# Performance work log

Hardware: AMD Instinct MI355X
Metric: run time of the kernel (lower is better)

The kernel has to match this reference:

```python
import jax, jax.numpy as jnp
import numpy as np

N, M, K, C, FF, H, OUT = 20000, 80000, 48, 64, 256, 4, 64


def _lin(x, w, b):
    return x @ w.T + b


def _bn(x, g, b, eps=1e-5):
    mu = x.mean(0)
    var = x.var(0)
    return (x - mu) * jax.lax.rsqrt(var + eps) * g + b


def setup_inputs() -> dict:
    key = jax.random.key(0)
    ks = jax.random.split(key, 24)
    voxel_features = jax.random.normal(ks[0], (M, C), jnp.float32)
    voxel_coords = jax.random.normal(ks[1], (M, 3), jnp.float32)
    query_coords = jax.random.normal(ks[2], (N, 3), jnp.float32)
    idx = jax.random.randint(ks[3], (N, K), 0, M)
    drop = jax.random.uniform(ks[4], (N, K)) < 0.1
    drop = drop.at[:, 0].set(False)  # keep >=1 valid key per query
    key_indices = jnp.where(drop, -1, idx)
    s = 0.05
    p = lambda i, shp: jax.random.normal(ks[i], shp, jnp.float32) * s
    return {
        "voxel_features": voxel_features,
        "voxel_coords": voxel_coords,
        "query_coords": query_coords,
        "key_indices": key_indices,
        "q_w": p(5, (C, 3)), "q_b": p(6, (C,)),
        "kpos_w": p(7, (C, 3)), "kpos_b": p(8, (C,)),
        "in_w": p(9, (3 * C, C)), "in_b": p(10, (3 * C,)),
        "out_w": p(11, (C, C)), "out_b": p(12, (C,)),
        "lin1_w": p(13, (FF, C)), "lin1_b": p(14, (FF,)),
        "lin2_w": p(15, (C, FF)), "lin2_b": p(16, (C,)),
        "norm_g": jnp.ones((C,), jnp.float32), "norm_b": jnp.zeros((C,), jnp.float32),
        "outl_w": p(17, (OUT, C)), "outl_b": p(18, (OUT,)),
        "obn_g": jnp.ones((OUT,), jnp.float32), "obn_b": jnp.zeros((OUT,), jnp.float32),
    }


def reference(voxel_features, voxel_coords, query_coords, key_indices,
              q_w, q_b, kpos_w, kpos_b, in_w, in_b, out_w, out_b,
              lin1_w, lin1_b, lin2_w, lin2_b, norm_g, norm_b,
              outl_w, outl_b, obn_g, obn_b):
    hd = C // H
    mask = key_indices < 0                      # (N,K) padded keys
    safe = jnp.where(mask, 0, key_indices)
    key_feats = voxel_features[safe]            # (N,K,C) hash-gather
    key_coords = voxel_coords[safe]             # (N,K,3)
    # query positional projection
    q_feat = jax.nn.relu(_lin(query_coords, q_w, q_b))          # (N,C)
    # relative coords + key positional conv1d(kernel=1) == linear on coord dim
    rel = key_coords - query_coords[:, None, :]                  # (N,K,3)
    key_feats = key_feats + jax.nn.relu(_lin(rel, kpos_w, kpos_b))
    # multihead attention, query length 1 per voxel
    Wq, Wk, Wv = jnp.split(in_w, 3, axis=0)
    bq, bk, bv = jnp.split(in_b, 3)
    q = (_lin(q_feat, Wq, bq) / jnp.sqrt(jnp.float32(hd))).reshape(N, H, hd)
    k = _lin(key_feats, Wk, bk).reshape(N, K, H, hd)
    v = _lin(key_feats, Wv, bv).reshape(N, K, H, hd)
    scores = jnp.einsum('nhd,nkhd->nhk', q, k)
    scores = jnp.where(mask[:, None, :], -jnp.inf, scores)
    attn = jax.nn.softmax(scores, axis=-1)
    ctx = jnp.einsum('nhk,nkhd->nhd', attn, v).reshape(N, C)
    att = _lin(ctx, out_w, out_b)                                # (N,C)
    # FFN + residual
    x = att + _lin(jax.nn.relu(_lin(att, lin1_w, lin1_b)), lin2_w, lin2_b)
    x = _bn(x, norm_g, norm_b)
    # output layer: Linear -> BN -> ReLU
    x = jax.nn.relu(_bn(_lin(x, outl_w, outl_b), obn_g, obn_b))
    return x
```

## Files before the change

### kernel.cpp

```cpp
#include <hip/hip_runtime.h>
#include <math.h>

#define N_Q 20000
#define KK 48
#define CC 64
#define FFD 256

#define TW_WOT   0
#define TW_WVT   4096
#define TW_L1B   8192
#define TW_L2B   16384
#define TW_OLB   24576
#define TW_QB    26624
#define TW_KB    28672
#define ST_OFF   32768
#define M_OFF    33024
#define VF_OFF   2593024

typedef short bf16x8 __attribute__((ext_vector_type(8)));
typedef float f32x4  __attribute__((ext_vector_type(4)));

__device__ __forceinline__ unsigned f2bf(float f) {
    unsigned u = __float_as_uint(f);
    return (u + 0x7fffu + ((u >> 16) & 1u)) >> 16;
}
__device__ __forceinline__ unsigned pk2(float a, float b) {
    return f2bf(a) | (f2bf(b) << 16);
}
__device__ __forceinline__ float bflo(unsigned u) { return __uint_as_float(u << 16); }
__device__ __forceinline__ float bfhi(unsigned u) { return __uint_as_float(u & 0xffff0000u); }
__device__ __forceinline__ bf16x8 ldfrag(const unsigned short* p) {
    return *(const bf16x8*)p;
}

__global__ void prep_all(const float* __restrict__ in_w,
                         const float* __restrict__ out_w,
                         const float* __restrict__ lin1_w,
                         const float* __restrict__ lin2_w,
                         const float* __restrict__ outl_w,
                         const float* __restrict__ vfeat,
                         float* __restrict__ tw,
                         unsigned short* __restrict__ vfeat_bf,
                         float* __restrict__ stats)
{
    int t = blockIdx.x * 256 + threadIdx.x;
    unsigned* twu = (unsigned*)tw;
    if (t < 1280000) {
        float4 v = ((const float4*)vfeat)[t];
        uint2 p; p.x = pk2(v.x, v.y); p.y = pk2(v.z, v.w);
        ((uint2*)vfeat_bf)[t] = p;
    }
    if (t < 256) stats[t] = 0.0f;
    if (t < 4096) {
        int c = t >> 6, j = t & 63;
        tw[TW_WOT + j*64 + c] = out_w[c*64 + j];
    } else if (t < 8192) {
        int i = t - 4096, cp = i >> 6, c = i & 63;
        tw[TW_WVT + cp*64 + c] = in_w[(128 + c)*64 + cp];
    } else if (t < 16384) {
        int p = t - 8192;
        int j2 = p & 3, lane = (p >> 2) & 63, nb = (p >> 8) & 15, ks = p >> 12;
        int n = nb*16 + (lane & 15), k = ks*32 + (lane >> 4)*8 + 2*j2;
        twu[TW_L1B + p] = pk2(lin1_w[n*64 + k], lin1_w[n*64 + k + 1]);
    } else if (t < 24576) {
        int p = t - 16384;
        int j2 = p & 3, lane = (p >> 2) & 63, nb = (p >> 8) & 3, ks = p >> 10;
        int n = nb*16 + (lane & 15), k = ks*32 + (lane >> 4)*8 + 2*j2;
        twu[TW_L2B + p] = pk2(lin2_w[n*256 + k], lin2_w[n*256 + k + 1]);
    } else if (t < 26624) {
        int p = t - 24576;
        int j2 = p & 3, lane = (p >> 2) & 63, nb = (p >> 8) & 3, ks = p >> 10;
        int n = nb*16 + (lane & 15), k = ks*32 + (lane >> 4)*8 + 2*j2;
        twu[TW_OLB + p] = pk2(outl_w[n*64 + k], outl_w[n*64 + k + 1]);
    } else if (t < 28672) {
        int p = t - 26624;
        int j2 = p & 3, lane = (p >> 2) & 63, nb = (p >> 8) & 3, ks = p >> 10;
        int n = nb*16 + (lane & 15), k = ks*32 + (lane >> 4)*8 + 2*j2;
        twu[TW_QB + p] = pk2(in_w[n*64 + k], in_w[n*64 + k + 1]);
    } else if (t < 32768) {
        int p = t - 28672;
        int j2 = p & 3, lane = (p >> 2) & 63, nb = (p >> 8) & 3, h = p >> 10;
        int j = nb*16 + (lane & 15), k = (lane >> 4)*8 + 2*j2;
        unsigned u = 0;
        if (k < 16)
            u = pk2(in_w[(64 + h*16 + k)*64 + j], in_w[(64 + h*16 + k + 1)*64 + j]);
        twu[TW_KB + p] = u;
    }
}

__global__ __launch_bounds__(256) void m_kernel(
    const float* __restrict__ qcoord, const float* __restrict__ q_w,
    const float* __restrict__ q_b, const float* __restrict__ in_b,
    const float* __restrict__ tw, unsigned short* __restrict__ M_all)
{
    __shared__ __align__(16) unsigned short sQF[80*72];
    __shared__ __align__(16) unsigned short sQ[80*72];
    int t = threadIdx.x, base = blockIdx.x * 80;
    int colq = (t*4) & 63;
    float qwv[12];
    #pragma unroll
    for (int j = 0; j < 12; ++j) qwv[j] = q_w[colq*3 + j];
    float4 qb4 = *(const float4*)&q_b[colq];
    #pragma unroll
    for (int i = 0; i < 5; ++i) {
        int e = i*1024 + t*4, r = e >> 6, n = base + r;
        float c0 = qcoord[n*3], c1 = qcoord[n*3+1], c2 = qcoord[n*3+2];
        float f0 = fmaxf(fmaf(qwv[2],  c2, fmaf(qwv[1],  c1, fmaf(qwv[0], c0, qb4.x))), 0.f);
        float f1 = fmaxf(fmaf(qwv[5],  c2, fmaf(qwv[4],  c1, fmaf(qwv[3], c0, qb4.y))), 0.f);
        float f2 = fmaxf(fmaf(qwv[8],  c2, fmaf(qwv[7],  c1, fmaf(qwv[6], c0, qb4.z))), 0.f);
        float f3 = fmaxf(fmaf(qwv[11], c2, fmaf(qwv[10], c1, fmaf(qwv[9], c0, qb4.w))), 0.f);
        uint2 p; p.x = pk2(f0, f1); p.y = pk2(f2, f3);
        *(uint2*)&sQF[r*72 + colq] = p;
    }
    int w = t >> 6, lane = t & 63, l16 = lane & 15, quad = lane >> 4;
    const unsigned* QB = (const unsigned*)(tw + TW_QB);
    const unsigned* KB = (const unsigned*)(tw + TW_KB);
    bf16x8 qbf[2], kbf[4];
    #pragma unroll
    for (int ks = 0; ks < 2; ++ks)
        qbf[ks] = ldfrag((const unsigned short*)&QB[((ks*4 + w)*64 + lane)*4]);
    #pragma unroll
    for (int nb = 0; nb < 4; ++nb)
        kbf[nb] = ldfrag((const unsigned short*)&KB[((w*4 + nb)*64 + lane)*4]);
    __syncthreads();

    int cq = w*16 + l16;
    float bq = in_b[cq];
    #pragma unroll
    for (int mb = 0; mb < 5; ++mb) {
        bf16x8 a0 = ldfrag(&sQF[(mb*16 + l16)*72 + quad*8]);
        bf16x8 a1 = ldfrag(&sQF[(mb*16 + l16)*72 + 32 + quad*8]);
        f32x4 acc = {0.f, 0.f, 0.f, 0.f};
        acc = __builtin_amdgcn_mfma_f32_16x16x32_bf16(a0, qbf[0], acc, 0, 0, 0);
        acc = __builtin_amdgcn_mfma_f32_16x16x32_bf16(a1, qbf[1], acc, 0, 0, 0);
        #pragma unroll
        for (int reg = 0; reg < 4; ++reg) {
            int row = mb*16 + quad*4 + reg;
            sQ[row*72 + cq] = (unsigned short)f2bf((acc[reg] + bq) * 0.25f);
        }
    }
    #pragma unroll
    for (int mb = 0; mb < 5; ++mb) {
        bf16x8 a = {0,0,0,0,0,0,0,0};
        if (quad < 2) a = ldfrag(&sQ[(mb*16 + l16)*72 + w*16 + quad*8]);
        f32x4 acc[4];
        #pragma unroll
        for (int nb = 0; nb < 4; ++nb) {
            f32x4 z = {0.f, 0.f, 0.f, 0.f};
            acc[nb] = __builtin_amdgcn_mfma_f32_16x16x32_bf16(a, kbf[nb], z, 0, 0, 0);
        }
        #pragma unroll
        for (int nb = 0; nb < 4; ++nb)
            #pragma unroll
            for (int reg = 0; reg < 4; ++reg) {
                int r = base + mb*16 + quad*4 + reg, j = nb*16 + l16;
                M_all[(size_t)r*256 + j*4 + w] = (unsigned short)f2bf(acc[nb][reg]);
            }
    }
}

__global__ __launch_bounds__(64, 4) void attn_kernel(
    const unsigned short* __restrict__ vfeat_bf, const float* __restrict__ vcoord,
    const float* __restrict__ qcoord, const int* __restrict__ kidx,
    const float* __restrict__ kpos_w, const float* __restrict__ kpos_b,
    const float* __restrict__ in_b, const float* __restrict__ out_b,
    const float* __restrict__ tw, const unsigned short* __restrict__ M_all,
    float* __restrict__ att_out)
{
    __shared__ __align__(16) unsigned short skf[KK*72];
    __shared__ __align__(16) float reg1[256];
    int n = blockIdx.x, c = threadIdx.x;
    int l16 = c & 15, h = c >> 4;
    float* sM   = reg1;
    float* sP   = reg1;
    float* sctx = reg1 + 192;
    float* sT   = (float*)skf;

    {
        uint2 mu = ((const uint2*)(M_all + (size_t)n*256))[c];
        float4 mf;
        mf.x = bflo(mu.x); mf.y = bfhi(mu.x);
        mf.z = bflo(mu.y); mf.w = bfhi(mu.y);
        *(float4*)&sM[4*c] = mf;
    }

    float qc0 = qcoord[n*3+0], qc1 = qcoord[n*3+1], qc2 = qcoord[n*3+2];

    int kread = c < 48 ? c : 47;
    int idxv = kidx[(size_t)n*KK + kread];
    int sfe = idxv < 0 ? 0 : idxv;
    float rl0 = vcoord[sfe*3+0] - qc0;
    float rl1 = vcoord[sfe*3+1] - qc1;
    float rl2 = vcoord[sfe*3+2] - qc2;

    float4 wA  = *(const float4*)(kpos_w + 12*l16 + 0);
    float4 wB  = *(const float4*)(kpos_w + 12*l16 + 4);
    float4 wC  = *(const float4*)(kpos_w + 12*l16 + 8);
    float4 kb4 = *(const float4*)(kpos_b + 4*l16);

    uint2 fv[12];
    #pragma unroll
    for (int i = 0; i < 12; ++i) {
        int row = 4*i + h;
        int si = __shfl(idxv, row);
        si = si < 0 ? 0 : si;
        fv[i] = *(const uint2*)(vfeat_bf + (size_t)si*64 + 4*l16);
    }
    #pragma unroll
    for (int i = 0; i < 12; ++i) {
        int row = 4*i + h;
        float rr0 = __shfl(rl0, row), rr1 = __shfl(rl1, row), rr2 = __shfl(rl2, row);
        float g0 = bflo(fv[i].x), g1 = bfhi(fv[i].x);
        float g2 = bflo(fv[i].y), g3 = bfhi(fv[i].y);
        g0 += fmaxf(fmaf(wA.x, rr0, fmaf(wA.y, rr1, fmaf(wA.z, rr2, kb4.x))), 0.0f);
        g1 += fmaxf(fmaf(wA.w, rr0, fmaf(wB.x, rr1, fmaf(wB.y, rr2, kb4.y))), 0.0f);
        g2 += fmaxf(fmaf(wB.z, rr0, fmaf(wB.w, rr1, fmaf(wC.x, rr2, kb4.z))), 0.0f);
        g3 += fmaxf(fmaf(wC.y, rr0, fmaf(wC.z, rr1, fmaf(wC.w, rr2, kb4.w))), 0.0f);
        uint2 p; p.x = pk2(g0, g1); p.y = pk2(g2, g3);
        *(uint2*)&skf[row*72 + 4*l16] = p;
    }

    int i0 = __shfl(idxv, l16), i1 = __shfl(idxv, l16 + 16), i2 = __shfl(idxv, l16 + 32);
    float S0 = 0, S1 = 0, S2 = 0;
    #pragma unroll
    for (int j8 = 0; j8 < 8; ++j8) {
        uint2 A = *(const uint2*)&skf[ l16       *72 + 8*j8];
        uint2 A2= *(const uint2*)&skf[ l16       *72 + 8*j8 + 4];
        uint2 B = *(const uint2*)&skf[(l16 + 16) *72 + 8*j8];
        uint2 B2= *(const uint2*)&skf[(l16 + 16) *72 + 8*j8 + 4];
        uint2 D = *(const uint2*)&skf[(l16 + 32) *72 + 8*j8];
        uint2 D2= *(const uint2*)&skf[(l16 + 32) *72 + 8*j8 + 4];
        #pragma unroll
        for (int jj = 0; jj < 8; ++jj) {
            unsigned ua = (jj < 4) ? ((jj < 2) ? A.x : A.y) : ((jj < 6) ? A2.x : A2.y);
            unsigned ub = (jj < 4) ? ((jj < 2) ? B.x : B.y) : ((jj < 6) ? B2.x : B2.y);
            unsigned ud = (jj < 4) ? ((jj < 2) ? D.x : D.y) : ((jj < 6) ? D2.x : D2.y);
            float av = (jj & 1) ? bfhi(ua) : bflo(ua);
            float bv = (jj & 1) ? bfhi(ub) : bflo(ub);
            float dv = (jj & 1) ? bfhi(ud) : bflo(ud);
            float m  = sM[(8*j8 + jj)*4 + h];
            S0 = fmaf(av, m, S0);
            S1 = fmaf(bv, m, S1);
            S2 = fmaf(dv, m, S2);
        }
    }
    if (i0 < 0) S0 = -INFINITY;
    if (i1 < 0) S1 = -INFINITY;
    if (i2 < 0) S2 = -INFINITY;

    float mx = fmaxf(S0, fmaxf(S1, S2));
    #pragma unroll
    for (int off = 8; off >= 1; off >>= 1) mx = fmaxf(mx, __shfl_xor(mx, off, 16));
    float e0 = __expf(S0 - mx), e1 = __expf(S1 - mx), e2 = __expf(S2 - mx);
    float es = e0 + e1 + e2;
    #pragma unroll
    for (int off = 8; off >= 1; off >>= 1) es += __shfl_xor(es, off, 16);
    float rinv = 1.0f / es;
    sP[ l16       *4 + h] = e0 * rinv;
    sP[(l16 + 16) *4 + h] = e1 * rinv;
    sP[(l16 + 32) *4 + h] = e2 * rinv;

    float T0 = 0, T1 = 0, T2 = 0, T3 = 0;
    #pragma unroll 8
    for (int k = 0; k < KK; ++k) {
        float kf = __uint_as_float(((unsigned)skf[k*72 + c]) << 16);
        float4 p = *(const float4*)&sP[k*4];
        T0 = fmaf(p.x, kf, T0); T1 = fmaf(p.y, kf, T1);
        T2 = fmaf(p.z, kf, T2); T3 = fmaf(p.w, kf, T3);
    }
    sT[0*65 + c] = T0; sT[1*65 + c] = T1; sT[2*65 + c] = T2; sT[3*65 + c] = T3;

    const float* WvT = tw + TW_WVT;
    float ctx = in_b[128 + c];
    #pragma unroll 8
    for (int cp = 0; cp < 64; ++cp)
        ctx = fmaf(sT[h*65 + cp], WvT[cp*64 + c], ctx);
    sctx[c] = ctx;

    const float* WoT = tw + TW_WOT;
    float att = out_b[c];
    #pragma unroll 8
    for (int j = 0; j < 64; ++j)
        att = fmaf(sctx[j], WoT[j*64 + c], att);
    att_out[(size_t)n*64 + c] = att;
}

__global__ __launch_bounds__(256) void ffn_kernel(
    const float* __restrict__ tw, const float* __restrict__ lin1_b,
    const float* __restrict__ lin2_b, float* __restrict__ att_y,
    float* __restrict__ sum1, float* __restrict__ sumsq1)
{
    __shared__ __align__(16) unsigned short sA[80*72];
    __shared__ __align__(16) unsigned short sH[80*264];
    int t = threadIdx.x, base = blockIdx.x * 80;
    #pragma unroll
    for (int i = 0; i < 5; ++i) {
        int e = i*1024 + t*4, r = e >> 6, col = e & 63;
        float4 v = *(const float4*)&att_y[(size_t)(base + r)*64 + col];
        uint2 p; p.x = pk2(v.x, v.y); p.y = pk2(v.z, v.w);
        *(uint2*)&sA[r*72 + col] = p;
    }
    int w = t >> 6, lane = t & 63, l16 = lane & 15, quad = lane >> 4;
    const unsigned* L1B = (const unsigned*)(tw + TW_L1B);
    const unsigned* L2B = (const unsigned*)(tw + TW_L2B);
    bf16x8 b1f[2][4], b2f[8];
    #pragma unroll
    for (int ks = 0; ks < 2; ++ks)
        #pragma unroll
        for (int nb = 0; nb < 4; ++nb)
            b1f[ks][nb] = ldfrag((const unsigned short*)&L1B[((ks*16 + w*4 + nb)*64 + lane)*4]);
    #pragma unroll
    for (int ks = 0; ks < 8; ++ks)
        b2f[ks] = ldfrag((const unsigned short*)&L2B[((ks*4 + w)*64 + lane)*4]);
    __syncthreads();

    #pragma unroll
    for (int mb = 0; mb < 5; ++mb) {
        bf16x8 a0 = ldfrag(&sA[(mb*16 + l16)*72 + quad*8]);
        bf16x8 a1 = ldfrag(&sA[(mb*16 + l16)*72 + 32 + quad*8]);
        #pragma unroll
        for (int nb = 0; nb < 4; ++nb) {
            f32x4 acc = {0.f, 0.f, 0.f, 0.f};
            acc = __builtin_amdgcn_mfma_f32_16x16x32_bf16(a0, b1f[0][nb], acc, 0, 0, 0);
            acc = __builtin_amdgcn_mfma_f32_16x16x32_bf16(a1, b1f[1][nb], acc, 0, 0, 0);
            int f = w*64 + nb*16 + l16;
            float bias = lin1_b[f];
            #pragma unroll
            for (int reg = 0; reg < 4; ++reg) {
                int row = mb*16 + quad*4 + reg;
                sH[row*264 + f] = (unsigned short)f2bf(fmaxf(acc[reg] + bias, 0.0f));
            }
        }
    }
    __syncthreads();

    int c = w*16 + l16;
    float lb2 = lin2_b[c];
    float s = 0.f, ss = 0.f;
    #pragma unroll
    for (int mb = 0; mb < 5; ++mb) {
        f32x4 acc = {0.f, 0.f, 0.f, 0.f};
        #pragma unroll
        for (int ks = 0; ks < 8; ++ks) {
            bf16x8 a = ldfrag(&sH[(mb*16 + l16)*264 + ks*32 + quad*8]);
            acc = __builtin_amdgcn_mfma_f32_16x16x32_bf16(a, b2f[ks], acc, 0, 0, 0);
        }
        #pragma unroll
        for (int reg = 0; reg < 4; ++reg) {
            int r = base + mb*16 + quad*4 + reg;
            float y = att_y[(size_t)r*64 + c] + lb2 + acc[reg];
            att_y[(size_t)r*64 + c] = y;
            s += y; ss = fmaf(y, y, ss);
        }
    }
    s  += __shfl_xor(s, 16);  s  += __shfl_xor(s, 32);
    ss += __shfl_xor(ss, 16); ss += __shfl_xor(ss, 32);
    if (lane < 16) {
        atomicAdd(&sum1[c], s);
        atomicAdd(&sumsq1[c], ss);
    }
}

__global__ __launch_bounds__(256) void linout_kernel(
    const float* __restrict__ tw, const float* __restrict__ outl_b,
    const float* __restrict__ norm_g, const float* __restrict__ norm_b,
    const float* __restrict__ sum1, const float* __restrict__ sumsq1,
    const float* __restrict__ y, float* __restrict__ z_out,
    float* __restrict__ sum2, float* __restrict__ sumsq2)
{
    __shared__ __align__(16) unsigned short sX[80*72];
    int t = threadIdx.x, base = blockIdx.x * 80;
    int colq = (t*4) & 63;
    const float invN = 1.0f / 20000.0f;
    float4 sm = *(const float4*)&sum1[colq];
    float4 sq = *(const float4*)&sumsq1[colq];
    float4 g  = *(const float4*)&norm_g[colq];
    float4 bb = *(const float4*)&norm_b[colq];
    float mu0 = sm.x*invN, mu1 = sm.y*invN, mu2 = sm.z*invN, mu3 = sm.w*invN;
    float a0 = g.x / sqrtf(fmaf(-mu0, mu0, sq.x*invN) + 1e-5f);
    float a1 = g.y / sqrtf(fmaf(-mu1, mu1, sq.y*invN) + 1e-5f);
    float a2 = g.z / sqrtf(fmaf(-mu2, mu2, sq.z*invN) + 1e-5f);
    float a3 = g.w / sqrtf(fmaf(-mu3, mu3, sq.w*invN) + 1e-5f);
    float b0 = fmaf(-mu0, a0, bb.x), b1 = fmaf(-mu1, a1, bb.y);
    float b2 = fmaf(-mu2, a2, bb.z), b3 = fmaf(-mu3, a3, bb.w);
    #pragma unroll
    for (int i = 0; i < 5; ++i) {
        int e = i*1024 + t*4, r = e >> 6;
        float4 v = *(const float4*)&y[(size_t)(base + r)*64 + colq];
        uint2 p;
        p.x = pk2(fmaf(v.x, a0, b0), fmaf(v.y, a1, b1));
        p.y = pk2(fmaf(v.z, a2, b2), fmaf(v.w, a3, b3));
        *(uint2*)&sX[r*72 + colq] = p;
    }
    int w = t >> 6, lane = t & 63, l16 = lane & 15, quad = lane >> 4;
    const unsigned* OLB = (const unsigned*)(tw + TW_OLB);
    bf16x8 obf[2];
    #pragma unroll
    for (int ks = 0; ks < 2; ++ks)
        obf[ks] = ldfrag((const unsigned short*)&OLB[((ks*4 + w)*64 + lane)*4]);
    __syncthreads();

    int co = w*16 + l16;
    float ob = outl_b[co];
    float s = 0.f, ss = 0.f;
    #pragma unroll
    for (int mb = 0; mb < 5; ++mb) {
        bf16x8 x0 = ldfrag(&sX[(mb*16 + l16)*72 + quad*8]);
        bf16x8 x1 = ldfrag(&sX[(mb*16 + l16)*72 + 32 + quad*8]);
        f32x4 acc = {0.f, 0.f, 0.f, 0.f};
        acc = __builtin_amdgcn_mfma_f32_16x16x32_bf16(x0, obf[0], acc, 0, 0, 0);
        acc = __builtin_amdgcn_mfma_f32_16x16x32_bf16(x1, obf[1], acc, 0, 0, 0);
        #pragma unroll
        for (int reg = 0; reg < 4; ++reg) {
            int r = base + mb*16 + quad*4 + reg;
            float zv = acc[reg] + ob;
            z_out[(size_t)r*64 + co] = zv;
            s += zv; ss = fmaf(zv, zv, ss);
        }
    }
    s  += __shfl_xor(s, 16);  s  += __shfl_xor(s, 32);
    ss += __shfl_xor(ss, 16); ss += __shfl_xor(ss, 32);
    if (lane < 16) {
        atomicAdd(&sum2[co], s);
        atomicAdd(&sumsq2[co], ss);
    }
}

__global__ void final_kernel(float* __restrict__ z,
    const float* __restrict__ sum2, const float* __restrict__ sumsq2,
    const float* __restrict__ obn_g, const float* __restrict__ obn_b)
{
    int i = blockIdx.x*blockDim.x + threadIdx.x;
    if (i >= N_Q*64/4) return;
    int o4 = (i*4) & 63;
    float4 sm = *(const float4*)&sum2[o4];
    float4 sq = *(const float4*)&sumsq2[o4];
    float4 g  = *(const float4*)&obn_g[o4];
    float4 b  = *(const float4*)&obn_b[o4];
    const float invN = 1.0f / 20000.0f;
    float mux = sm.x*invN, muy = sm.y*invN, muz = sm.z*invN, muw = sm.w*invN;
    float ax = g.x / sqrtf(fmaf(-mux, mux, sq.x*invN) + 1e-5f);
    float ay = g.y / sqrtf(fmaf(-muy, muy, sq.y*invN) + 1e-5f);
    float az = g.z / sqrtf(fmaf(-muz, muz, sq.z*invN) + 1e-5f);
    float aw = g.w / sqrtf(fmaf(-muw, muw, sq.w*invN) + 1e-5f);
    float4 v = ((float4*)z)[i];
    v.x = fmaxf(fmaf(v.x - mux, ax, b.x), 0.0f);
    v.y = fmaxf(fmaf(v.y - muy, ay, b.y), 0.0f);
    v.z = fmaxf(fmaf(v.z - muz, az, b.z), 0.0f);
    v.w = fmaxf(fmaf(v.w - muw, aw, b.w), 0.0f);
    ((float4*)z)[i] = v;
}

extern "C" void kernel_launch(void* const* d_in, const int* in_sizes, int n_in,
                              void* d_out, int out_size, void* d_ws, size_t ws_size,
                              hipStream_t stream)
{
    const float* vfeat  = (const float*)d_in[0];
    const float* vcoord = (const float*)d_in[1];
    const float* qcoord = (const float*)d_in[2];
    const int*   kidx   = (const int*)d_in[3];
    const float* q_w    = (const float*)d_in[4];
    const float* q_b    = (const float*)d_in[5];
    const float* kpos_w = (const float*)d_in[6];
    const float* kpos_b = (const float*)d_in[7];
    const float* in_w   = (const float*)d_in[8];
    const float* in_b   = (const float*)d_in[9];
    const float* out_w  = (const float*)d_in[10];
    const float* out_b  = (const float*)d_in[11];
    const float* lin1_w = (const float*)d_in[12];
    const float* lin1_b = (const float*)d_in[13];
    const float* lin2_w = (const float*)d_in[14];
    const float* lin2_b = (const float*)d_in[15];
    const float* norm_g = (const float*)d_in[16];
    const float* norm_b = (const float*)d_in[17];
    const float* outl_w = (const float*)d_in[18];
    const float* outl_b = (const float*)d_in[19];
    const float* obn_g  = (const float*)d_in[20];
    const float* obn_b  = (const float*)d_in[21];

    float* ws = (float*)d_ws;
    float* tw = ws;
    float* stats = ws + ST_OFF;
    float* sum1 = stats, *sumsq1 = stats + 64, *sum2 = stats + 128, *sumsq2 = stats + 192;
    unsigned short* M_all = (unsigned short*)(ws + M_OFF);
    unsigned short* vfeat_bf = (unsigned short*)(ws + VF_OFF);
    float* xd = (float*)d_out;

    prep_all<<<5120, 256, 0, stream>>>(in_w, out_w, lin1_w, lin2_w, outl_w,
                                       vfeat, tw, vfeat_bf, stats);
    m_kernel<<<250, 256, 0, stream>>>(qcoord, q_w, q_b, in_b, tw, M_all);
    attn_kernel<<<N_Q, 64, 0, stream>>>(vfeat_bf, vcoord, qcoord, kidx, kpos_w, kpos_b,
                                        in_b, out_b, tw, M_all, xd);
    ffn_kernel<<<250, 256, 0, stream>>>(tw, lin1_b, lin2_b, xd, sum1, sumsq1);
    linout_kernel<<<250, 256, 0, stream>>>(tw, outl_b, norm_g, norm_b, sum1, sumsq1,
                                           xd, xd, sum2, sumsq2);
    final_kernel<<<1250, 256, 0, stream>>>(xd, sum2, sumsq2, obn_g, obn_b);
}
```

Measured before the change: 203.1 us.

## Store weights row-major bf16, relayout M for vector loads, shrink FFN tiles

Weights are now stored as plain row-major bf16 in the workspace, so the MFMA fragments are read directly with row/k indexing instead of being pre-swizzled into per-lane fragment order. The M_all layout changes to head-major so attn_kernel can read the per-head M values as float4 vectors from shared memory instead of scalar strided loads. The FFN and linout kernels drop from 80 to 48 rows per block (417 blocks) with tail guards, which should raise the number of blocks on the CUs. The catch is slightly less coalesced fragment loads and extra bounds checks.

```diff
diff --git a/kernel.cpp b/kernel.cpp
--- a/kernel.cpp
+++ b/kernel.cpp
@@ -8,11 +8,11 @@
 
 #define TW_WOT   0
 #define TW_WVT   4096
-#define TW_L1B   8192
-#define TW_L2B   16384
-#define TW_OLB   24576
-#define TW_QB    26624
-#define TW_KB    28672
+#define U_L1     16384
+#define U_L2     32768
+#define U_OL     49152
+#define U_WQ     53248
+#define U_WK     57344
 #define ST_OFF   32768
 #define M_OFF    33024
 #define VF_OFF   2593024
@@ -40,58 +40,51 @@
                          const float* __restrict__ outl_w,
                          const float* __restrict__ vfeat,
                          float* __restrict__ tw,
+                         unsigned short* __restrict__ wsu,
                          unsigned short* __restrict__ vfeat_bf,
                          float* __restrict__ stats)
 {
     int t = blockIdx.x * 256 + threadIdx.x;
-    unsigned* twu = (unsigned*)tw;
     if (t < 1280000) {
         float4 v = ((const float4*)vfeat)[t];
         uint2 p; p.x = pk2(v.x, v.y); p.y = pk2(v.z, v.w);
         ((uint2*)vfeat_bf)[t] = p;
-    }
-    if (t < 256) stats[t] = 0.0f;
-    if (t < 4096) {
-        int c = t >> 6, j = t & 63;
+        return;
+    }
+    int u = t - 1280000;
+    if (u < 4096) {
+        int c = u >> 6, j = u & 63;
         tw[TW_WOT + j*64 + c] = out_w[c*64 + j];
-    } else if (t < 8192) {
-        int i = t - 4096, cp = i >> 6, c = i & 63;
+    } else if (u < 8192) {
+        int i = u - 4096, cp = i >> 6, c = i & 63;
         tw[TW_WVT + cp*64 + c] = in_w[(128 + c)*64 + cp];
-    } else if (t < 16384) {
-        int p = t - 8192;
-        int j2 = p & 3, lane = (p >> 2) & 63, nb = (p >> 8) & 15, ks = p >> 12;
-        int n = nb*16 + (lane & 15), k = ks*32 + (lane >> 4)*8 + 2*j2;
-        twu[TW_L1B + p] = pk2(lin1_w[n*64 + k], lin1_w[n*64 + k + 1]);
-    } else if (t < 24576) {
-        int p = t - 16384;
-        int j2 = p & 3, lane = (p >> 2) & 63, nb = (p >> 8) & 3, ks = p >> 10;
-        int n = nb*16 + (lane & 15), k = ks*32 + (lane >> 4)*8 + 2*j2;
-        twu[TW_L2B + p] = pk2(lin2_w[n*256 + k], lin2_w[n*256 + k + 1]);
-    } else if (t < 26624) {
-        int p = t - 24576;
-        int j2 = p & 3, lane = (p >> 2) & 63, nb = (p >> 8) & 3, ks = p >> 10;
-        int n = nb*16 + (lane & 15), k = ks*32 + (lane >> 4)*8 + 2*j2;
-        twu[TW_OLB + p] = pk2(outl_w[n*64 + k], outl_w[n*64 + k + 1]);
-    } else if (t < 28672) {
-        int p = t - 26624;
-        int j2 = p & 3, lane = (p >> 2) & 63, nb = (p >> 8) & 3, ks = p >> 10;
-        int n = nb*16 + (lane & 15), k = ks*32 + (lane >> 4)*8 + 2*j2;
-        twu[TW_QB + p] = pk2(in_w[n*64 + k], in_w[n*64 + k + 1]);
-    } else if (t < 32768) {
-        int p = t - 28672;
-        int j2 = p & 3, lane = (p >> 2) & 63, nb = (p >> 8) & 3, h = p >> 10;
-        int j = nb*16 + (lane & 15), k = (lane >> 4)*8 + 2*j2;
-        unsigned u = 0;
-        if (k < 16)
-            u = pk2(in_w[(64 + h*16 + k)*64 + j], in_w[(64 + h*16 + k + 1)*64 + j]);
-        twu[TW_KB + p] = u;
+    } else if (u < 24576) {
+        int i = u - 8192;
+        wsu[U_L1 + i] = (unsigned short)f2bf(lin1_w[i]);
+    } else if (u < 40960) {
+        int i = u - 24576;
+        wsu[U_L2 + i] = (unsigned short)f2bf(lin2_w[i]);
+    } else if (u < 45056) {
+        int i = u - 40960;
+        wsu[U_OL + i] = (unsigned short)f2bf(outl_w[i]);
+    } else if (u < 49152) {
+        int i = u - 45056;
+        wsu[U_WQ + i] = (unsigned short)f2bf(in_w[i]);
+    } else if (u < 57344) {
+        int v = u - 49152;
+        int h = v >> 11, rem = v & 2047, j = rem >> 5, k = rem & 31;
+        unsigned short val = 0;
+        if (k < 16) val = (unsigned short)f2bf(in_w[(64 + h*16 + k)*64 + j]);
+        wsu[U_WK + v] = val;
+    } else if (u < 57600) {
+        stats[u - 57344] = 0.0f;
     }
 }
 
 __global__ __launch_bounds__(256) void m_kernel(
     const float* __restrict__ qcoord, const float* __restrict__ q_w,
     const float* __restrict__ q_b, const float* __restrict__ in_b,
-    const float* __restrict__ tw, unsigned short* __restrict__ M_all)
+    const unsigned short* __restrict__ wsu, unsigned short* __restrict__ M_all)
 {
     __shared__ __align__(16) unsigned short sQF[80*72];
     __shared__ __align__(16) unsigned short sQ[80*72];
@@ -113,15 +106,13 @@
         *(uint2*)&sQF[r*72 + colq] = p;
     }
     int w = t >> 6, lane = t & 63, l16 = lane & 15, quad = lane >> 4;
-    const unsigned* QB = (const unsigned*)(tw + TW_QB);
-    const unsigned* KB = (const unsigned*)(tw + TW_KB);
     bf16x8 qbf[2], kbf[4];
     #pragma unroll
     for (int ks = 0; ks < 2; ++ks)
-        qbf[ks] = ldfrag((const unsigned short*)&QB[((ks*4 + w)*64 + lane)*4]);
+        qbf[ks] = ldfrag(&wsu[U_WQ + (w*16 + l16)*64 + ks*32 + quad*8]);
     #pragma unroll
     for (int nb = 0; nb < 4; ++nb)
-        kbf[nb] = ldfrag((const unsigned short*)&KB[((w*4 + nb)*64 + lane)*4]);
+        kbf[nb] = ldfrag(&wsu[U_WK + w*2048 + (nb*16 + l16)*32 + quad*8]);
     __syncthreads();
 
     int cq = w*16 + l16;
@@ -154,7 +145,7 @@
             #pragma unroll
             for (int reg = 0; reg < 4; ++reg) {
                 int r = base + mb*16 + quad*4 + reg, j = nb*16 + l16;
-                M_all[(size_t)r*256 + j*4 + w] = (unsigned short)f2bf(acc[nb][reg]);
+                M_all[(size_t)r*256 + w*64 + j] = (unsigned short)f2bf(acc[nb][reg]);
             }
     }
 }
@@ -181,7 +172,7 @@
         float4 mf;
         mf.x = bflo(mu.x); mf.y = bfhi(mu.x);
         mf.z = bflo(mu.y); mf.w = bfhi(mu.y);
-        *(float4*)&sM[4*c] = mf;
+        *(float4*)&sM[h*64 + 4*l16] = mf;
     }
 
     float qc0 = qcoord[n*3+0], qc1 = qcoord[n*3+1], qc2 = qcoord[n*3+2];
@@ -230,6 +221,8 @@
         uint2 B2= *(const uint2*)&skf[(l16 + 16) *72 + 8*j8 + 4];
         uint2 D = *(const uint2*)&skf[(l16 + 32) *72 + 8*j8];
         uint2 D2= *(const uint2*)&skf[(l16 + 32) *72 + 8*j8 + 4];
+        float4 mA = *(const float4*)&sM[h*64 + 8*j8];
+        float4 mB = *(const float4*)&sM[h*64 + 8*j8 + 4];
         #pragma unroll
         for (int jj = 0; jj < 8; ++jj) {
             unsigned ua = (jj < 4) ? ((jj < 2) ? A.x : A.y) : ((jj < 6) ? A2.x : A2.y);
@@ -238,7 +231,8 @@
             float av = (jj & 1) ? bfhi(ua) : bflo(ua);
             float bv = (jj & 1) ? bfhi(ub) : bflo(ub);
             float dv = (jj & 1) ? bfhi(ud) : bflo(ud);
-            float m  = sM[(8*j8 + jj)*4 + h];
+            float m  = (jj < 4) ? ((jj < 2) ? ((jj & 1) ? mA.y : mA.x) : ((jj & 1) ? mA.w : mA.z))
+                                : ((jj < 6) ? ((jj & 1) ? mB.y : mB.x) : ((jj & 1) ? mB.w : mB.z));
             S0 = fmaf(av, m, S0);
             S1 = fmaf(bv, m, S1);
             S2 = fmaf(dv, m, S2);
@@ -286,36 +280,38 @@
 }
 
 __global__ __launch_bounds__(256) void ffn_kernel(
-    const float* __restrict__ tw, const float* __restrict__ lin1_b,
+    const unsigned short* __restrict__ wsu, const float* __restrict__ lin1_b,
     const float* __restrict__ lin2_b, float* __restrict__ att_y,
     float* __restrict__ sum1, float* __restrict__ sumsq1)
 {
-    __shared__ __align__(16) unsigned short sA[80*72];
-    __shared__ __align__(16) unsigned short sH[80*264];
-    int t = threadIdx.x, base = blockIdx.x * 80;
-    #pragma unroll
-    for (int i = 0; i < 5; ++i) {
+    __shared__ __align__(16) unsigned short sA[48*72];
+    __shared__ __align__(16) unsigned short sH[48*264];
+    int t = threadIdx.x, base = blockIdx.x * 48;
+    #pragma unroll
+    for (int i = 0; i < 3; ++i) {
         int e = i*1024 + t*4, r = e >> 6, col = e & 63;
-        float4 v = *(const float4*)&att_y[(size_t)(base + r)*64 + col];
-        uint2 p; p.x = pk2(v.x, v.y); p.y = pk2(v.z, v.w);
+        int n = base + r;
+        uint2 p = {0u, 0u};
+        if (n < N_Q) {
+            float4 v = *(const float4*)&att_y[(size_t)n*64 + col];
+            p.x = pk2(v.x, v.y); p.y = pk2(v.z, v.w);
+        }
         *(uint2*)&sA[r*72 + col] = p;
     }
     int w = t >> 6, lane = t & 63, l16 = lane & 15, quad = lane >> 4;
-    const unsigned* L1B = (const unsigned*)(tw + TW_L1B);
-    const unsigned* L2B = (const unsigned*)(tw + TW_L2B);
     bf16x8 b1f[2][4], b2f[8];
     #pragma unroll
     for (int ks = 0; ks < 2; ++ks)
         #pragma unroll
         for (int nb = 0; nb < 4; ++nb)
-            b1f[ks][nb] = ldfrag((const unsigned short*)&L1B[((ks*16 + w*4 + nb)*64 + lane)*4]);
+            b1f[ks][nb] = ldfrag(&wsu[U_L1 + (w*64 + nb*16 + l16)*64 + ks*32 + quad*8]);
     #pragma unroll
     for (int ks = 0; ks < 8; ++ks)
-        b2f[ks] = ldfrag((const unsigned short*)&L2B[((ks*4 + w)*64 + lane)*4]);
+        b2f[ks] = ldfrag(&wsu[U_L2 + (w*16 + l16)*256 + ks*32 + quad*8]);
     __syncthreads();
 
     #pragma unroll
-    for (int mb = 0; mb < 5; ++mb) {
+    for (int mb = 0; mb < 3; ++mb) {
         bf16x8 a0 = ldfrag(&sA[(mb*16 + l16)*72 + quad*8]);
         bf16x8 a1 = ldfrag(&sA[(mb*16 + l16)*72 + 32 + quad*8]);
         #pragma unroll
@@ -338,7 +334,7 @@
     float lb2 = lin2_b[c];
     float s = 0.f, ss = 0.f;
     #pragma unroll
-    for (int mb = 0; mb < 5; ++mb) {
+    for (int mb = 0; mb < 3; ++mb) {
         f32x4 acc = {0.f, 0.f, 0.f, 0.f};
         #pragma unroll
         for (int ks = 0; ks < 8; ++ks) {
@@ -348,9 +344,11 @@
         #pragma unroll
         for (int reg = 0; reg < 4; ++reg) {
             int r = base + mb*16 + quad*4 + reg;
-            float y = att_y[(size_t)r*64 + c] + lb2 + acc[reg];
-            att_y[(size_t)r*64 + c] = y;
-            s += y; ss = fmaf(y, y, ss);
+            if (r < N_Q) {
+                float y = att_y[(size_t)r*64 + c] + lb2 + acc[reg];
+                att_y[(size_t)r*64 + c] = y;
+                s += y; ss = fmaf(y, y, ss);
+            }
         }
     }
     s  += __shfl_xor(s, 16);  s  += __shfl_xor(s, 32);
@@ -362,14 +360,14 @@
 }
 
 __global__ __launch_bounds__(256) void linout_kernel(
-    const float* __restrict__ tw, const float* __restrict__ outl_b,
+    const unsigned short* __restrict__ wsu, const float* __restrict__ outl_b,
     const float* __restrict__ norm_g, const float* __restrict__ norm_b,
     const float* __restrict__ sum1, const float* __restrict__ sumsq1,
     const float* __restrict__ y, float* __restrict__ z_out,
     float* __restrict__ sum2, float* __restrict__ sumsq2)
 {
-    __shared__ __align__(16) unsigned short sX[80*72];
-    int t = threadIdx.x, base = blockIdx.x * 80;
+    __shared__ __align__(16) unsigned short sX[48*72];
+    int t = threadIdx.x, base = blockIdx.x * 48;
     int colq = (t*4) & 63;
     const float invN = 1.0f / 20000.0f;
     float4 sm = *(const float4*)&sum1[colq];
@@ -384,27 +382,29 @@
     float b0 = fmaf(-mu0, a0, bb.x), b1 = fmaf(-mu1, a1, bb.y);
     float b2 = fmaf(-mu2, a2, bb.z), b3 = fmaf(-mu3, a3, bb.w);
     #pragma unroll
-    for (int i = 0; i < 5; ++i) {
+    for (int i = 0; i < 3; ++i) {
         int e = i*1024 + t*4, r = e >> 6;
-        float4 v = *(const float4*)&y[(size_t)(base + r)*64 + colq];
-        uint2 p;
-        p.x = pk2(fmaf(v.x, a0, b0), fmaf(v.y, a1, b1));
-        p.y = pk2(fmaf(v.z, a2, b2), fmaf(v.w, a3, b3));
+        int n = base + r;
+        uint2 p = {0u, 0u};
+        if (n < N_Q) {
+            float4 v = *(const float4*)&y[(size_t)n*64 + colq];
+            p.x = pk2(fmaf(v.x, a0, b0), fmaf(v.y, a1, b1));
+            p.y = pk2(fmaf(v.z, a2, b2), fmaf(v.w, a3, b3));
+        }
         *(uint2*)&sX[r*72 + colq] = p;
     }
     int w = t >> 6, lane = t & 63, l16 = lane & 15, quad = lane >> 4;
-    const unsigned* OLB = (const unsigned*)(tw + TW_OLB);
     bf16x8 obf[2];
     #pragma unroll
     for (int ks = 0; ks < 2; ++ks)
-        obf[ks] = ldfrag((const unsigned short*)&OLB[((ks*4 + w)*64 + lane)*4]);
+        obf[ks] = ldfrag(&wsu[U_OL + (w*16 + l16)*64 + ks*32 + quad*8]);
     __syncthreads();
 
     int co = w*16 + l16;
     float ob = outl_b[co];
     float s = 0.f, ss = 0.f;
     #pragma unroll
-    for (int mb = 0; mb < 5; ++mb) {
+    for (int mb = 0; mb < 3; ++mb) {
         bf16x8 x0 = ldfrag(&sX[(mb*16 + l16)*72 + quad*8]);
         bf16x8 x1 = ldfrag(&sX[(mb*16 + l16)*72 + 32 + quad*8]);
         f32x4 acc = {0.f, 0.f, 0.f, 0.f};
@@ -413,9 +413,11 @@
         #pragma unroll
         for (int reg = 0; reg < 4; ++reg) {
             int r = base + mb*16 + quad*4 + reg;
-            float zv = acc[reg] + ob;
-            z_out[(size_t)r*64 + co] = zv;
-            s += zv; ss = fmaf(zv, zv, ss);
+            if (r < N_Q) {
+                float zv = acc[reg] + ob;
+                z_out[(size_t)r*64 + co] = zv;
+                s += zv; ss = fmaf(zv, zv, ss);
+            }
         }
     }
     s  += __shfl_xor(s, 16);  s  += __shfl_xor(s, 32);
@@ -480,19 +482,20 @@
 
     float* ws = (float*)d_ws;
     float* tw = ws;
+    unsigned short* wsu = (unsigned short*)ws;
     float* stats = ws + ST_OFF;
     float* sum1 = stats, *sumsq1 = stats + 64, *sum2 = stats + 128, *sumsq2 = stats + 192;
     unsigned short* M_all = (unsigned short*)(ws + M_OFF);
     unsigned short* vfeat_bf = (unsigned short*)(ws + VF_OFF);
     float* xd = (float*)d_out;
 
-    prep_all<<<5120, 256, 0, stream>>>(in_w, out_w, lin1_w, lin2_w, outl_w,
-                                       vfeat, tw, vfeat_bf, stats);
-    m_kernel<<<250, 256, 0, stream>>>(qcoord, q_w, q_b, in_b, tw, M_all);
+    prep_all<<<5225, 256, 0, stream>>>(in_w, out_w, lin1_w, lin2_w, outl_w,
+                                       vfeat, tw, wsu, vfeat_bf, stats);
+    m_kernel<<<250, 256, 0, stream>>>(qcoord, q_w, q_b, in_b, wsu, M_all);
     attn_kernel<<<N_Q, 64, 0, stream>>>(vfeat_bf, vcoord, qcoord, kidx, kpos_w, kpos_b,
                                         in_b, out_b, tw, M_all, xd);
-    ffn_kernel<<<250, 256, 0, stream>>>(tw, lin1_b, lin2_b, xd, sum1, sumsq1);
-    linout_kernel<<<250, 256, 0, stream>>>(tw, outl_b, norm_g, norm_b, sum1, sumsq1,
+    ffn_kernel<<<417, 256, 0, stream>>>(wsu, lin1_b, lin2_b, xd, sum1, sumsq1);
+    linout_kernel<<<417, 256, 0, stream>>>(wsu, outl_b, norm_g, norm_b, sum1, sumsq1,
                                            xd, xd, sum2, sumsq2);
     final_kernel<<<1250, 256, 0, stream>>>(xd, sum2, sumsq2, obn_g, obn_b);
 }
```

New measurement: 208.6 us. 2.7% more time.
